# Optimization experiments

Hardware: AMD Instinct MI355X
Metric: run time of the kernel (lower is better)

## Reference

```python
import jax, jax.numpy as jnp
import numpy as np

B, L, KD, ED, H = 8, 4096, 512, 1024, 8  # batch, seq, key_dim, embed_dim, n_heads
LN_EPS = 1e-5


def setup_inputs() -> dict:
    key = jax.random.key(0)
    ks = jax.random.split(key, 6)
    keys = jax.random.normal(ks[0], (B, L, KD), dtype=jnp.float32)
    values = jax.random.normal(ks[1], (B, L, ED), dtype=jnp.float32)
    # learned params
    query = jax.random.normal(ks[2], (H, 1, KD // H), dtype=jnp.float32) * 0.02
    k_bias = jax.random.normal(ks[3], (KD,), dtype=jnp.float32) / np.sqrt(KD).astype(np.float32)
    v_bias = jnp.zeros((ED,), dtype=jnp.float32)
    softmax_weight = 1.0 + 0.01 * jax.random.normal(ks[4], (H, 1, L + 1), dtype=jnp.float32)
    softmax_bias = 0.01 * jax.random.normal(ks[5], (H, 1, L + 1), dtype=jnp.float32)
    gamma = jnp.ones((ED,), dtype=jnp.float32)
    beta = jnp.zeros((ED,), dtype=jnp.float32)
    return {"keys": keys, "values": values, "query": query, "k_bias": k_bias,
            "v_bias": v_bias, "softmax_weight": softmax_weight,
            "softmax_bias": softmax_bias, "gamma": gamma, "beta": beta}


def reference(keys, values, query, k_bias, v_bias, softmax_weight, softmax_bias, gamma, beta):
    b = keys.shape[0]
    # append learned bias token to keys and values  -> [B, L+1, *]
    keys = jnp.concatenate([keys, jnp.broadcast_to(k_bias, (b, 1, k_bias.shape[0]))], axis=1)
    values = jnp.concatenate([values, jnp.broadcast_to(v_bias, (b, 1, v_bias.shape[0]))], axis=1)
    lp = keys.shape[1]
    # torch multihead_reshape is a raw contiguous view [B,L,C] -> [B*H, L, C/H]
    K = keys.reshape(b * H, lp, keys.shape[2] // H)      # [B*H, L+1, KD/H]
    V = values.reshape(b * H, lp, values.shape[2] // H)  # [B*H, L+1, ED/H]
    Q = jnp.tile(query, (b, 1, 1))                       # [B*H, 1, KD/H]
    scores = jnp.einsum('bqd,bld->bql', Q, K)            # [B*H, 1, L+1]
    scores = scores * jnp.tile(softmax_weight, (b, 1, 1)) + jnp.tile(softmax_bias, (b, 1, 1))
    attn = jax.nn.softmax(scores, axis=-1)               # [B*H, 1, L+1]
    A = jnp.einsum('bql,bld->bqd', attn, V)              # [B*H, 1, ED/H]
    A = A.reshape(b, 1, -1)                              # multihead_unshape -> [B, 1, ED]
    # LayerNorm over embed dim (torch default eps=1e-5, biased var)
    mean = jnp.mean(A, axis=-1, keepdims=True)
    var = jnp.var(A, axis=-1, keepdims=True)
    return (A - mean) * jax.lax.rsqrt(var + LN_EPS) * gamma + beta
```

## Files before the change

### kernel.cpp

```cpp
#include <hip/hip_runtime.h>

#define BATCH 8
#define LSEQ  4096
#define LP    4097
#define KDIM  512
#define EDIM  1024
#define NH    8
#define DK    64
#define DV    128
#define NG    64
#define NC    32
#define RC    129
#define LN_EPS 1e-5f

typedef float floatx4 __attribute__((ext_vector_type(4)));

__global__ __launch_bounds__(256) void lqa_fused_kernel(
    const float* __restrict__ keys, const float* __restrict__ k_bias,
    const float* __restrict__ values, const float* __restrict__ v_bias,
    const float* __restrict__ query, const float* __restrict__ sw,
    const float* __restrict__ sb, float* __restrict__ partials,
    float2* __restrict__ stats)
{
    const int chunk = blockIdx.x;
    const int g = blockIdx.y;
    const int b = g >> 3, h = g & 7;
    const int t = threadIdx.x;
    const int lane16 = t & 15;
    const int d0k = lane16 * 4;

    const int row0 = chunk * RC;
    const int nrows = min(LP, row0 + RC) - row0;

    __shared__ float ts[RC];
    __shared__ float red1[256];
    __shared__ float red4[256 * 4];

    const floatx4 q = *reinterpret_cast<const floatx4*>(query + h * DK + d0k);
    const float* kp = keys + (long long)b * (LSEQ * KDIM);
    const int fheadk = h * (LP * DK);
    const float* w = sw + h * LP;
    const float* bb = sb + h * LP;

    float mloc = -1e30f;
    for (int r = (t >> 4); r < nrows; r += 16) {
        const int row = row0 + r;
        const int f = fheadk + row * DK + d0k;
        const floatx4 k = (f < LSEQ * KDIM)
            ? *reinterpret_cast<const floatx4*>(kp + f)
            : *reinterpret_cast<const floatx4*>(k_bias + (f - LSEQ * KDIM));
        float s = q.x * k.x + q.y * k.y + q.z * k.z + q.w * k.w;
        s += __shfl_xor(s, 1);
        s += __shfl_xor(s, 2);
        s += __shfl_xor(s, 4);
        s += __shfl_xor(s, 8);
        if (lane16 == 0) {
            const float tv = s * w[row] + bb[row];
            ts[r] = tv;
            mloc = fmaxf(mloc, tv);
        }
    }
    red1[t] = mloc;
    for (int off = 128; off > 0; off >>= 1) {
        __syncthreads();
        if (t < off) red1[t] = fmaxf(red1[t], red1[t + off]);
    }
    __syncthreads();
    const float mc = red1[0];
    __syncthreads();

    float zloc = 0.f;
    for (int r = t; r < nrows; r += 256) {
        const float e = __expf(ts[r] - mc);
        ts[r] = e;
        zloc += e;
    }
    red1[t] = zloc;
    for (int off = 128; off > 0; off >>= 1) {
        __syncthreads();
        if (t < off) red1[t] += red1[t + off];
    }
    __syncthreads();
    const float zc = red1[0];

    const int srow = t >> 5;
    const int d0v = (t & 31) * 4;
    const float* vp = values + (long long)b * (LSEQ * EDIM);
    const int fheadv = h * (LP * DV);

    float acc[4] = {0.f, 0.f, 0.f, 0.f};
    for (int r = srow; r < nrows; r += 8) {
        const float wgt = ts[r];
        const int f = fheadv + (row0 + r) * DV + d0v;
        const floatx4 v = (f < LSEQ * EDIM)
            ? *reinterpret_cast<const floatx4*>(vp + f)
            : *reinterpret_cast<const floatx4*>(v_bias + (f - LSEQ * EDIM));
        acc[0] += wgt * v.x; acc[1] += wgt * v.y;
        acc[2] += wgt * v.z; acc[3] += wgt * v.w;
    }

#pragma unroll
    for (int j = 0; j < 4; ++j) red4[t * 4 + j] = acc[j];
    for (int off = 128; off >= 32; off >>= 1) {
        __syncthreads();
        if (t < off) {
#pragma unroll
            for (int j = 0; j < 4; ++j) red4[t * 4 + j] += red4[(t + off) * 4 + j];
        }
    }
    __syncthreads();
    if (t < 32) {
        float* dst = partials + ((long long)(g * NC + chunk)) * DV + t * 4;
#pragma unroll
        for (int j = 0; j < 4; ++j) dst[j] = red4[t * 4 + j];
    }
    if (t == 0) stats[g * NC + chunk] = make_float2(mc, zc);
}

__global__ __launch_bounds__(256) void lqa_combine_ln_kernel(
    const float* __restrict__ partials, const float2* __restrict__ stats,
    const float* __restrict__ gamma, const float* __restrict__ beta,
    float* __restrict__ out)
{
    const int b = blockIdx.x;
    const int t = threadIdx.x;
    __shared__ float mh[NH], zh[NH];
    __shared__ float wc[NH * NC];
    __shared__ float r1[256], r2[256];

    if (t < NH) {
        const float2* st = stats + (b * NH + t) * NC;
        float m = -1e30f, Z = 0.f;
#pragma unroll
        for (int c = 0; c < NC; ++c) {
            const float2 s = st[c];
            const float mn = fmaxf(m, s.x);
            Z = Z * __expf(m - mn) + s.y * __expf(s.x - mn);
            m = mn;
        }
        mh[t] = m; zh[t] = Z;
    }
    __syncthreads();
    {
        const int h = t >> 5, c = t & 31;
        const float2 s = stats[(b * NH + h) * NC + c];
        wc[t] = __expf(s.x - mh[h]) / zh[h];
    }
    __syncthreads();

    float a[4];
    float s1 = 0.f, s2 = 0.f;
#pragma unroll
    for (int i = 0; i < 4; ++i) {
        const int e = t + i * 256;
        const int h = e >> 7, d = e & 127;
        const float* src = partials + ((long long)((b * NH + h) * NC)) * DV + d;
        const float* wr = wc + h * NC;
        float sum = 0.f;
#pragma unroll
        for (int c = 0; c < NC; ++c) sum += src[c * DV] * wr[c];
        a[i] = sum;
        s1 += sum;
        s2 += sum * sum;
    }
    r1[t] = s1; r2[t] = s2; __syncthreads();
    for (int off = 128; off > 0; off >>= 1) {
        if (t < off) { r1[t] += r1[t + off]; r2[t] += r2[t + off]; }
        __syncthreads();
    }
    const float mean = r1[0] * (1.0f / EDIM);
    const float var = r2[0] * (1.0f / EDIM) - mean * mean;
    const float inv = rsqrtf(var + LN_EPS);
#pragma unroll
    for (int i = 0; i < 4; ++i) {
        const int e = t + i * 256;
        out[(long long)b * EDIM + e] = (a[i] - mean) * inv * gamma[e] + beta[e];
    }
}

extern "C" void kernel_launch(void* const* d_in, const int* in_sizes, int n_in,
                              void* d_out, int out_size, void* d_ws, size_t ws_size,
                              hipStream_t stream) {
    const float* keys   = (const float*)d_in[0];
    const float* values = (const float*)d_in[1];
    const float* query  = (const float*)d_in[2];
    const float* k_bias = (const float*)d_in[3];
    const float* v_bias = (const float*)d_in[4];
    const float* sw     = (const float*)d_in[5];
    const float* sb     = (const float*)d_in[6];
    const float* gamma  = (const float*)d_in[7];
    const float* beta   = (const float*)d_in[8];
    float* out = (float*)d_out;

    float* ws = (float*)d_ws;
    float* partials = ws;
    float2* stats = (float2*)(ws + (long long)NG * NC * DV);

    lqa_fused_kernel<<<dim3(NC, NG), 256, 0, stream>>>(
        keys, k_bias, values, v_bias, query, sw, sb, partials, stats);
    lqa_combine_ln_kernel<<<BATCH, 256, 0, stream>>>(
        partials, stats, gamma, beta, out);
}
```

Baseline: 258.4 us.

## Prefetch value rows into registers and use wave-shuffle reductions

```diff
diff --git a/kernel.cpp b/kernel.cpp
--- a/kernel.cpp
+++ b/kernel.cpp
@@ -11,11 +11,12 @@
 #define NG    64
 #define NC    32
 #define RC    129
+#define RPAD  144
 #define LN_EPS 1e-5f
 
 typedef float floatx4 __attribute__((ext_vector_type(4)));
 
-__global__ __launch_bounds__(256) void lqa_fused_kernel(
+__global__ __launch_bounds__(256, 3) void lqa_fused_kernel(
     const float* __restrict__ keys, const float* __restrict__ k_bias,
     const float* __restrict__ values, const float* __restrict__ v_bias,
     const float* __restrict__ query, const float* __restrict__ sw,
@@ -26,16 +27,32 @@
     const int g = blockIdx.y;
     const int b = g >> 3, h = g & 7;
     const int t = threadIdx.x;
+    const int wave = t >> 6;
+    const int lane = t & 63;
+
+    const int row0 = chunk * RC;
+    const int nrows = min(LP, row0 + RC) - row0;
+
+    __shared__ float ts[RPAD];
+    __shared__ float red1[8];
+    __shared__ float red2[4 * 128];
+
+    const int srow = t >> 5;
+    const int d0v = (t & 31) * 4;
+    const float* vp = values + (long long)b * (LSEQ * EDIM);
+    const int fheadv = h * (LP * DV);
+    floatx4 vreg[17];
+#pragma unroll
+    for (int k = 0; k < 17; ++k) {
+        const int row = min(row0 + srow + 8 * k, LP - 1);
+        const int f = fheadv + row * DV + d0v;
+        vreg[k] = (f < LSEQ * EDIM)
+            ? *reinterpret_cast<const floatx4*>(vp + f)
+            : *reinterpret_cast<const floatx4*>(v_bias + (f - LSEQ * EDIM));
+    }
+
     const int lane16 = t & 15;
     const int d0k = lane16 * 4;
-
-    const int row0 = chunk * RC;
-    const int nrows = min(LP, row0 + RC) - row0;
-
-    __shared__ float ts[RC];
-    __shared__ float red1[256];
-    __shared__ float red4[256 * 4];
-
     const floatx4 q = *reinterpret_cast<const floatx4*>(query + h * DK + d0k);
     const float* kp = keys + (long long)b * (LSEQ * KDIM);
     const int fheadk = h * (LP * DK);
@@ -43,76 +60,62 @@
     const float* bb = sb + h * LP;
 
     float mloc = -1e30f;
-    for (int r = (t >> 4); r < nrows; r += 16) {
-        const int row = row0 + r;
+#pragma unroll
+    for (int kk = 0; kk < 9; ++kk) {
+        const int r = (t >> 4) + 16 * kk;
+        const int row = min(row0 + r, LP - 1);
         const int f = fheadk + row * DK + d0k;
-        const floatx4 k = (f < LSEQ * KDIM)
+        const floatx4 kv = (f < LSEQ * KDIM)
             ? *reinterpret_cast<const floatx4*>(kp + f)
             : *reinterpret_cast<const floatx4*>(k_bias + (f - LSEQ * KDIM));
-        float s = q.x * k.x + q.y * k.y + q.z * k.z + q.w * k.w;
+        float s = q.x * kv.x + q.y * kv.y + q.z * kv.z + q.w * kv.w;
         s += __shfl_xor(s, 1);
         s += __shfl_xor(s, 2);
         s += __shfl_xor(s, 4);
         s += __shfl_xor(s, 8);
         if (lane16 == 0) {
-            const float tv = s * w[row] + bb[row];
+            const float tv = (r < nrows) ? s * w[row] + bb[row] : -1e30f;
             ts[r] = tv;
             mloc = fmaxf(mloc, tv);
         }
     }
-    red1[t] = mloc;
-    for (int off = 128; off > 0; off >>= 1) {
-        __syncthreads();
-        if (t < off) red1[t] = fmaxf(red1[t], red1[t + off]);
-    }
-    __syncthreads();
-    const float mc = red1[0];
-    __syncthreads();
+#pragma unroll
+    for (int off = 1; off < 64; off <<= 1)
+        mloc = fmaxf(mloc, __shfl_xor(mloc, off));
+    if (lane == 0) red1[wave] = mloc;
+    __syncthreads();
+    const float mc = fmaxf(fmaxf(red1[0], red1[1]), fmaxf(red1[2], red1[3]));
 
     float zloc = 0.f;
-    for (int r = t; r < nrows; r += 256) {
-        const float e = __expf(ts[r] - mc);
-        ts[r] = e;
-        zloc += e;
-    }
-    red1[t] = zloc;
-    for (int off = 128; off > 0; off >>= 1) {
-        __syncthreads();
-        if (t < off) red1[t] += red1[t + off];
-    }
-    __syncthreads();
-    const float zc = red1[0];
-
-    const int srow = t >> 5;
-    const int d0v = (t & 31) * 4;
-    const float* vp = values + (long long)b * (LSEQ * EDIM);
-    const int fheadv = h * (LP * DV);
+    if (t < RPAD) {
+        const float e = __expf(ts[t] - mc);
+        ts[t] = e;
+        zloc = e;
+    }
+#pragma unroll
+    for (int off = 1; off < 64; off <<= 1)
+        zloc += __shfl_xor(zloc, off);
+    if (lane == 0) red1[4 + wave] = zloc;
+    __syncthreads();
+    const float zc = red1[4] + red1[5] + red1[6] + red1[7];
 
     float acc[4] = {0.f, 0.f, 0.f, 0.f};
-    for (int r = srow; r < nrows; r += 8) {
-        const float wgt = ts[r];
-        const int f = fheadv + (row0 + r) * DV + d0v;
-        const floatx4 v = (f < LSEQ * EDIM)
-            ? *reinterpret_cast<const floatx4*>(vp + f)
-            : *reinterpret_cast<const floatx4*>(v_bias + (f - LSEQ * EDIM));
-        acc[0] += wgt * v.x; acc[1] += wgt * v.y;
-        acc[2] += wgt * v.z; acc[3] += wgt * v.w;
-    }
-
-#pragma unroll
-    for (int j = 0; j < 4; ++j) red4[t * 4 + j] = acc[j];
-    for (int off = 128; off >= 32; off >>= 1) {
-        __syncthreads();
-        if (t < off) {
-#pragma unroll
-            for (int j = 0; j < 4; ++j) red4[t * 4 + j] += red4[(t + off) * 4 + j];
-        }
-    }
-    __syncthreads();
-    if (t < 32) {
-        float* dst = partials + ((long long)(g * NC + chunk)) * DV + t * 4;
-#pragma unroll
-        for (int j = 0; j < 4; ++j) dst[j] = red4[t * 4 + j];
+#pragma unroll
+    for (int k = 0; k < 17; ++k) {
+        const float wgt = ts[srow + 8 * k];
+        acc[0] += wgt * vreg[k].x; acc[1] += wgt * vreg[k].y;
+        acc[2] += wgt * vreg[k].z; acc[3] += wgt * vreg[k].w;
+    }
+#pragma unroll
+    for (int j = 0; j < 4; ++j) acc[j] += __shfl_xor(acc[j], 32);
+    if (lane < 32) {
+#pragma unroll
+        for (int j = 0; j < 4; ++j) red2[wave * 128 + lane * 4 + j] = acc[j];
+    }
+    __syncthreads();
+    if (t < 128) {
+        const float sum = red2[t] + red2[128 + t] + red2[256 + t] + red2[384 + t];
+        partials[((long long)(g * NC + chunk)) * DV + t] = sum;
     }
     if (t == 0) stats[g * NC + chunk] = make_float2(mc, zc);
 }
```

After: 260.9 us. Within noise of the previous version (+0.9%).
